# Kernel optimization log

Hardware: AMD Instinct MI355X
Metric: run time of the kernel (lower is better)

## Reference

```python
import jax, jax.numpy as jnp
import numpy as np

H = 16
D = 64
EPS = 1e-6

def _phi(x):
    # elu_feature_map: elu(x) + 1
    return jax.nn.elu(x) + 1.0

def setup_inputs() -> dict:
    key = jax.random.key(0)
    k1, k2, k3, k4 = jax.random.split(key, 4)
    B, N = 4, 4096
    query = jax.random.normal(k1, (B, N, H * D), dtype=jnp.float32)
    key_t = jax.random.normal(k2, (B, N, H * D), dtype=jnp.float32)
    value = jax.random.normal(k3, (B, N, H * D), dtype=jnp.float32)
    W_out = jax.random.normal(k4, (D, H * D), dtype=jnp.float32) * (1.0 / np.sqrt(H * D))
    b_out = jnp.zeros((D,), dtype=jnp.float32)
    return {"query": query, "key": key_t, "value": value, "W_out": W_out, "b_out": b_out}

def reference(query, key, value, W_out, b_out):
    B, N, _ = query.shape
    # b n (h d) -> b h n d
    def split_heads(x):
        return x.reshape(B, N, H, D).transpose(0, 2, 1, 3)
    q = split_heads(query)
    k = split_heads(key)
    v = split_heads(value)
    Q = _phi(q)  # [B,H,N,D]
    K = _phi(k)
    # KV aggregation: O(N D^2)
    KV = jnp.einsum('bhnd,bhnm->bhdm', K, v)          # [B,H,D,D]
    Ksum = K.sum(axis=2)                               # [B,H,D]
    Z = 1.0 / (jnp.einsum('bhnd,bhd->bhn', Q, Ksum) + EPS)  # [B,H,N]
    out = jnp.einsum('bhnd,bhdm,bhn->bhnm', Q, KV, Z)  # [B,H,N,D]
    # b h n d -> b n h d -> (b*n, h*d)
    out = out.transpose(0, 2, 1, 3).reshape(B * N, H * D)
    return out @ W_out.T + b_out
```

## Files before the change

kernel.cpp:

```cpp
#include <hip/hip_runtime.h>

#define B_  4
#define N_  4096
#define H_  16
#define BH_ 64
#define S_  16
#define EPS_ 1e-6f

#define NST_ 40
#define TSZ_ 2560
#define KOST_ 72

typedef _Float16 h2  __attribute__((ext_vector_type(2)));
typedef _Float16 h8  __attribute__((ext_vector_type(8)));
typedef float    f4v __attribute__((ext_vector_type(4)));

struct H2x2 { h2 a, b; };
struct H2x4 { h2 e[4]; };

__device__ __forceinline__ h8 ld_h8(const _Float16* p) {
    f4v r = *(const f4v*)p;
    return __builtin_bit_cast(h8, r);
}
__device__ __forceinline__ H2x4 ld_h2x4(const _Float16* p) {
    f4v r = *(const f4v*)p;
    return __builtin_bit_cast(H2x4, r);
}
__device__ __forceinline__ void st_h2x2(_Float16* p, h2 a, h2 b) {
    H2x2 t{a, b};
    *(float2*)p = __builtin_bit_cast(float2, t);
}
__device__ __forceinline__ float phi(float x) {
    return x > 0.0f ? x + 1.0f : __expf(x);
}
__device__ __forceinline__ float fdot2(h2 a, h2 b, float c) {
    return __builtin_amdgcn_fdot2(a, b, c, false);
}

__global__ __launch_bounds__(256) void k_zero(float* __restrict__ p) {
    p[(size_t)blockIdx.x * 256 + threadIdx.x] = 0.f;
}

__global__ __launch_bounds__(256, 4) void k_kvpart(const float* __restrict__ K,
                                                   const float* __restrict__ V,
                                                   float* __restrict__ KV,
                                                   float* __restrict__ Ksum) {
    const int s = blockIdx.x, h = blockIdx.y, b = blockIdx.z;
    const int t = threadIdx.x, wv = t >> 6, lane = t & 63;
    const int rp2 = t >> 4, c4 = t & 15;
    const int l15 = lane & 15;

    __shared__ __align__(16) _Float16 pool[2 * 2 * TSZ_];

    f4v k0r, k1r, v0r, v1r;
    const float* baseK = K + ((size_t)(b * N_ + s * 256) * 1024 + h * 64 + c4 * 4);
    const float* baseV = V + ((size_t)(b * N_ + s * 256) * 1024 + h * 64 + c4 * 4);

    auto LOADX = [&](int chunk) {
        const int ro = (chunk * 32 + 2 * rp2) * 1024;
        k0r = *(const f4v*)(baseK + ro);
        k1r = *(const f4v*)(baseK + ro + 1024);
        v0r = *(const f4v*)(baseV + ro);
        v1r = *(const f4v*)(baseV + ro + 1024);
    };
    auto STOREX = [&](int bf) {
        _Float16* Kt = pool + bf * (2 * TSZ_);
        _Float16* Vt = Kt + TSZ_;
        const int nn = 2 * rp2;
#pragma unroll
        for (int dj = 0; dj < 4; ++dj) {
            const int d = 4 * c4 + dj;
            h2 kk, vv;
            kk.x = (_Float16)phi(k0r[dj]); kk.y = (_Float16)phi(k1r[dj]);
            vv.x = (_Float16)v0r[dj];      vv.y = (_Float16)v1r[dj];
            *(h2*)&Kt[d * NST_ + nn] = kk;
            *(h2*)&Vt[d * NST_ + nn] = vv;
        }
    };

    f4v acc[4];
#pragma unroll
    for (int j = 0; j < 4; ++j) acc[j] = (f4v){0.f, 0.f, 0.f, 0.f};
    float ksum = 0.f;
    h2 one2; one2.x = (_Float16)1.0f; one2.y = (_Float16)1.0f;
    const int fo = (lane >> 4) * 8;

    auto COMPUTE = [&](int bf) {
        const _Float16* Kt = pool + bf * (2 * TSZ_);
        const _Float16* Vt = Kt + TSZ_;
        h8 a0 = ld_h8(&Kt[(16 * wv + l15) * NST_ + fo]);
#pragma unroll
        for (int j = 0; j < 4; ++j) {
            h8 b0 = ld_h8(&Vt[(16 * j + l15) * NST_ + fo]);
            acc[j] = __builtin_amdgcn_mfma_f32_16x16x32_f16(a0, b0, acc[j], 0, 0, 0);
        }
        if (wv == 0) {
#pragma unroll
            for (int q = 0; q < 4; ++q) {
                H2x4 x = ld_h2x4(&Kt[lane * NST_ + q * 8]);
#pragma unroll
                for (int i = 0; i < 4; ++i) ksum = fdot2(x.e[i], one2, ksum);
            }
        }
    };

    LOADX(0);
    STOREX(0);
    __syncthreads();
#pragma unroll
    for (int c = 0; c < 8; ++c) {
        if (c < 7) LOADX(c + 1);
        COMPUTE(c & 1);
        if (c < 7) {
            STOREX((c + 1) & 1);
            __syncthreads();
        }
    }

    const int bh = b * 16 + h;
    float* outp = KV + (size_t)bh * 4096;
#pragma unroll
    for (int j = 0; j < 4; ++j)
#pragma unroll
        for (int r = 0; r < 4; ++r) {
            const int d = 16 * wv + (lane >> 4) * 4 + r;
            const int m = 16 * j + l15;
            atomicAdd(&outp[d * 64 + m], acc[j][r]);
        }
    if (wv == 0) atomicAdd(&Ksum[(size_t)bh * 64 + lane], ksum);
}

__global__ __launch_bounds__(256, 4) void k_makeM(const float* __restrict__ KV,
                                                  const float* __restrict__ W,
                                                  _Float16* __restrict__ Mt) {
    const int bh = blockIdx.x, dq = blockIdx.y;
    const int h  = bh & 15;
    const int t  = threadIdx.x;

    __shared__ float KVs[16][68];
    __shared__ float Ws[64][68];

    const f4v* kv4 = (const f4v*)KV;
    const f4v* W4  = (const f4v*)W;

    {
        const int row = t >> 4, c4 = t & 15;
        *(f4v*)&KVs[row][c4 * 4] = kv4[(size_t)bh * 1024 + (dq * 16 + row) * 16 + c4];
    }
    for (int idx = t; idx < 1024; idx += 256) {
        const int wrow = idx >> 4, wc = idx & 15;
        *(f4v*)&Ws[wrow][wc * 4] = W4[(size_t)wrow * 256 + h * 16 + wc];
    }
    __syncthreads();

    const int j = t >> 2, dl = (t & 3) * 4;
    float acc[4] = {0.f, 0.f, 0.f, 0.f};
#pragma unroll 4
    for (int m4 = 0; m4 < 16; ++m4) {
        f4v wr  = *(const f4v*)&Ws[j][m4 * 4];
        f4v kv0 = *(const f4v*)&KVs[dl + 0][m4 * 4];
        f4v kv1 = *(const f4v*)&KVs[dl + 1][m4 * 4];
        f4v kv2 = *(const f4v*)&KVs[dl + 2][m4 * 4];
        f4v kv3 = *(const f4v*)&KVs[dl + 3][m4 * 4];
        acc[0] += wr[0] * kv0[0] + wr[1] * kv0[1] + wr[2] * kv0[2] + wr[3] * kv0[3];
        acc[1] += wr[0] * kv1[0] + wr[1] * kv1[1] + wr[2] * kv1[2] + wr[3] * kv1[3];
        acc[2] += wr[0] * kv2[0] + wr[1] * kv2[1] + wr[2] * kv2[2] + wr[3] * kv2[3];
        acc[3] += wr[0] * kv3[0] + wr[1] * kv3[1] + wr[2] * kv3[2] + wr[3] * kv3[3];
    }
    h2 lo, hi;
    lo.x = (_Float16)acc[0]; lo.y = (_Float16)acc[1];
    hi.x = (_Float16)acc[2]; hi.y = (_Float16)acc[3];
    H2x2 pk{lo, hi};
    *(float2*)&Mt[((size_t)bh * 64 + j) * 64 + dq * 16 + dl] =
        __builtin_bit_cast(float2, pk);
}

__global__ __launch_bounds__(256, 4) void k_out(const float* __restrict__ Q,
                                                const _Float16* __restrict__ Mtg,
                                                const float* __restrict__ Ksum,
                                                const float* __restrict__ bout,
                                                float* __restrict__ out) {
    const int nc = blockIdx.x, b = blockIdx.y;
    const int n0 = nc * 16;
    const int t = threadIdx.x, wv = t >> 6, lane = t & 63;
    const int rp16 = t >> 4, c4 = t & 15, l15 = lane & 15;

    __shared__ __align__(16) _Float16 pool[2 * 80 * KOST_];
    __shared__ float zz[16];
    __shared__ h2 Kss[2][32];

    f4v qr, mr0, mr1;
    float ksa = 0.f, ksb = 0.f;
    auto LOAD = [&](int hh) {
        const int bh = b * 16 + hh;
        qr = *(const f4v*)(Q + ((size_t)(b * N_ + n0 + rp16) * 1024 + hh * 64 + c4 * 4));
        const f4v* gm = (const f4v*)(Mtg + (size_t)bh * 4096);
        mr0 = gm[t];
        mr1 = gm[t + 256];
        if (t < 32) {
            ksa = Ksum[(size_t)bh * 64 + 2 * t];
            ksb = Ksum[(size_t)bh * 64 + 2 * t + 1];
        }
    };
    auto STORE = [&](int bf) {
        _Float16* Qp = pool + bf * (80 * KOST_);
        _Float16* Mt = Qp + 16 * KOST_;
        h2 p0, p1;
        p0.x = (_Float16)phi(qr[0]); p0.y = (_Float16)phi(qr[1]);
        p1.x = (_Float16)phi(qr[2]); p1.y = (_Float16)phi(qr[3]);
        st_h2x2(&Qp[rp16 * KOST_ + 4 * c4], p0, p1);
        *(f4v*)&Mt[(t >> 3) * KOST_ + (t & 7) * 8] = mr0;
        *(f4v*)&Mt[((t + 256) >> 3) * KOST_ + (t & 7) * 8] = mr1;
        if (t < 32) { h2 kk; kk.x = (_Float16)ksa; kk.y = (_Float16)ksb; Kss[bf][t] = kk; }
    };

    const int fo = (lane >> 4) * 8;
    float facc[4] = {0.f, 0.f, 0.f, 0.f};

    LOAD(0);
    STORE(0);

    for (int hh = 0; hh < 16; ++hh) {
        if (hh + 1 < 16) LOAD(hh + 1);
        __syncthreads();
        const int bf = hh & 1;
        const _Float16* Qp = pool + bf * (80 * KOST_);
        const _Float16* Mt = Qp + 16 * KOST_;

        if (t < 16) {
            float zp = 0.f;
#pragma unroll
            for (int c = 0; c < 8; ++c) {
                H2x4 x = ld_h2x4(&Qp[t * KOST_ + c * 8]);
#pragma unroll
                for (int i = 0; i < 4; ++i) zp = fdot2(x.e[i], Kss[bf][c * 4 + i], zp);
            }
            zz[t] = 1.0f / (zp + EPS_);
        }
        __syncthreads();

        f4v acc = (f4v){0.f, 0.f, 0.f, 0.f};
#pragma unroll
        for (int ks = 0; ks < 2; ++ks) {
            h8 a0 = ld_h8(&Qp[l15 * KOST_ + ks * 32 + fo]);
            h8 b0 = ld_h8(&Mt[(16 * wv + l15) * KOST_ + ks * 32 + fo]);
            acc = __builtin_amdgcn_mfma_f32_16x16x32_f16(a0, b0, acc, 0, 0, 0);
        }
#pragma unroll
        for (int r = 0; r < 4; ++r) {
            const int row = (lane >> 4) * 4 + r;
            facc[r] += zz[row] * acc[r];
        }
        if (hh + 1 < 16) STORE((hh + 1) & 1);
    }

    const int j = 16 * wv + l15;
    const float bj = bout[j];
#pragma unroll
    for (int r = 0; r < 4; ++r) {
        const int n = n0 + (lane >> 4) * 4 + r;
        out[(size_t)(b * N_ + n) * 64 + j] = bj + facc[r];
    }
}

extern "C" void kernel_launch(void* const* d_in, const int* in_sizes, int n_in,
                              void* d_out, int out_size, void* d_ws, size_t ws_size,
                              hipStream_t stream) {
    const float* q  = (const float*)d_in[0];
    const float* k  = (const float*)d_in[1];
    const float* v  = (const float*)d_in[2];
    const float* W  = (const float*)d_in[3];
    const float* bo = (const float*)d_in[4];
    float* out = (float*)d_out;

    float* ws   = (float*)d_ws;
    float* KV   = ws;
    float* Ksum = KV + (size_t)BH_ * 4096;
    float* Mt   = Ksum + (size_t)BH_ * 64;

    k_zero<<<1040, 256, 0, stream>>>(KV);
    k_kvpart<<<dim3(S_, H_, B_), 256, 0, stream>>>(k, v, KV, Ksum);
    k_makeM<<<dim3(BH_, 4), 256, 0, stream>>>(KV, W, (_Float16*)Mt);
    k_out<<<dim3(N_ / 16, B_), 256, 0, stream>>>(q, (const _Float16*)Mt, Ksum, bo, out);
}
```

Baseline: 220.8 us.

## Fuse four kernels into one cooperative kernel with grid-wide syncs

```diff
diff --git a/kernel.cpp b/kernel.cpp
--- a/kernel.cpp
+++ b/kernel.cpp
@@ -1,4 +1,7 @@
 #include <hip/hip_runtime.h>
+#include <hip/hip_cooperative_groups.h>
+
+namespace cg = cooperative_groups;
 
 #define B_  4
 #define N_  4096
@@ -10,6 +13,7 @@
 #define NST_ 40
 #define TSZ_ 2560
 #define KOST_ 72
+#define POOLSZ_ (2 * 80 * KOST_)
 
 typedef _Float16 h2  __attribute__((ext_vector_type(2)));
 typedef _Float16 h8  __attribute__((ext_vector_type(8)));
@@ -37,20 +41,16 @@
     return __builtin_amdgcn_fdot2(a, b, c, false);
 }
 
-__global__ __launch_bounds__(256) void k_zero(float* __restrict__ p) {
-    p[(size_t)blockIdx.x * 256 + threadIdx.x] = 0.f;
-}
-
-__global__ __launch_bounds__(256, 4) void k_kvpart(const float* __restrict__ K,
-                                                   const float* __restrict__ V,
-                                                   float* __restrict__ KV,
-                                                   float* __restrict__ Ksum) {
-    const int s = blockIdx.x, h = blockIdx.y, b = blockIdx.z;
-    const int t = threadIdx.x, wv = t >> 6, lane = t & 63;
+
+__device__ __forceinline__ void phase_kvpart(int s, int h, int b, int t,
+                                             const float* __restrict__ K,
+                                             const float* __restrict__ V,
+                                             float* __restrict__ KV,
+                                             float* __restrict__ Ksum,
+                                             _Float16* pool) {
+    const int wv = t >> 6, lane = t & 63;
     const int rp2 = t >> 4, c4 = t & 15;
     const int l15 = lane & 15;
-
-    __shared__ __align__(16) _Float16 pool[2 * 2 * TSZ_];
 
     f4v k0r, k1r, v0r, v1r;
     const float* baseK = K + ((size_t)(b * N_ + s * 256) * 1024 + h * 64 + c4 * 4);
@@ -130,15 +130,14 @@
     if (wv == 0) atomicAdd(&Ksum[(size_t)bh * 64 + lane], ksum);
 }
 
-__global__ __launch_bounds__(256, 4) void k_makeM(const float* __restrict__ KV,
-                                                  const float* __restrict__ W,
-                                                  _Float16* __restrict__ Mt) {
-    const int bh = blockIdx.x, dq = blockIdx.y;
-    const int h  = bh & 15;
-    const int t  = threadIdx.x;
-
-    __shared__ float KVs[16][68];
-    __shared__ float Ws[64][68];
+__device__ __forceinline__ void phase_makeM(int bh, int dq, int t,
+                                            const float* __restrict__ KV,
+                                            const float* __restrict__ W,
+                                            _Float16* __restrict__ Mt,
+                                            float* fpool) {
+    float (*KVs)[68] = (float (*)[68])fpool;
+    float (*Ws)[68]  = (float (*)[68])(fpool + 16 * 68);
+    const int h = bh & 15;
 
     const f4v* kv4 = (const f4v*)KV;
     const f4v* W4  = (const f4v*)W;
@@ -175,19 +174,17 @@
         __builtin_bit_cast(float2, pk);
 }
 
-__global__ __launch_bounds__(256, 4) void k_out(const float* __restrict__ Q,
-                                                const _Float16* __restrict__ Mtg,
-                                                const float* __restrict__ Ksum,
-                                                const float* __restrict__ bout,
-                                                float* __restrict__ out) {
-    const int nc = blockIdx.x, b = blockIdx.y;
+__device__ __forceinline__ void phase_out(int nc, int b, int t,
+                                          const float* __restrict__ Q,
+                                          const _Float16* __restrict__ Mtg,
+                                          const float* __restrict__ Ksum,
+                                          const float* __restrict__ bout,
+                                          float* __restrict__ out,
+                                          _Float16* pool, float* zz,
+                                          h2 (*Kss)[32]) {
     const int n0 = nc * 16;
-    const int t = threadIdx.x, wv = t >> 6, lane = t & 63;
+    const int wv = t >> 6, lane = t & 63;
     const int rp16 = t >> 4, c4 = t & 15, l15 = lane & 15;
-
-    __shared__ __align__(16) _Float16 pool[2 * 80 * KOST_];
-    __shared__ float zz[16];
-    __shared__ h2 Kss[2][32];
 
     f4v qr, mr0, mr1;
     float ksa = 0.f, ksb = 0.f;
@@ -263,6 +260,65 @@
     }
 }
 
+__global__ __launch_bounds__(256, 4) void k_fused(const float* __restrict__ K,
+                                                  const float* __restrict__ V,
+                                                  const float* __restrict__ Q,
+                                                  const float* __restrict__ W,
+                                                  const float* __restrict__ bout,
+                                                  float* __restrict__ out,
+                                                  float* __restrict__ KV,
+                                                  float* __restrict__ Ksum,
+                                                  _Float16* __restrict__ Mt) {
+    const int bid = blockIdx.x;
+    const int t = threadIdx.x;
+    cg::grid_group grid = cg::this_grid();
+
+    __shared__ __align__(16) _Float16 pool[POOLSZ_];
+    __shared__ float zz[16];
+    __shared__ h2 Kss[2][32];
+
+    for (int idx = bid * 256 + t; idx < BH_ * 4096 + BH_ * 64; idx += 1024 * 256)
+        KV[idx] = 0.f;
+    grid.sync();
+
+    phase_kvpart(bid & 15, (bid >> 4) & 15, bid >> 8, t, K, V, KV, Ksum, pool);
+    __threadfence();
+    grid.sync();
+
+    if (bid < 256) phase_makeM(bid >> 2, bid & 3, t, KV, W, Mt, (float*)pool);
+    __threadfence();
+    grid.sync();
+
+    phase_out(bid & 255, bid >> 8, t, Q, Mt, Ksum, bout, out, pool, zz, Kss);
+}
+
+__global__ __launch_bounds__(256) void k_zero(float* __restrict__ p) {
+    p[(size_t)blockIdx.x * 256 + threadIdx.x] = 0.f;
+}
+__global__ __launch_bounds__(256, 4) void k_kvpart(const float* __restrict__ K,
+                                                   const float* __restrict__ V,
+                                                   float* __restrict__ KV,
+                                                   float* __restrict__ Ksum) {
+    __shared__ __align__(16) _Float16 pool[2 * 2 * TSZ_];
+    phase_kvpart(blockIdx.x, blockIdx.y, blockIdx.z, threadIdx.x, K, V, KV, Ksum, pool);
+}
+__global__ __launch_bounds__(256, 4) void k_makeM(const float* __restrict__ KV,
+                                                  const float* __restrict__ W,
+                                                  _Float16* __restrict__ Mt) {
+    __shared__ __align__(16) float fpool[80 * 68];
+    phase_makeM(blockIdx.x, blockIdx.y, threadIdx.x, KV, W, Mt, fpool);
+}
+__global__ __launch_bounds__(256, 4) void k_out(const float* __restrict__ Q,
+                                                const _Float16* __restrict__ Mtg,
+                                                const float* __restrict__ Ksum,
+                                                const float* __restrict__ bout,
+                                                float* __restrict__ out) {
+    __shared__ __align__(16) _Float16 pool[POOLSZ_];
+    __shared__ float zz[16];
+    __shared__ h2 Kss[2][32];
+    phase_out(blockIdx.x, blockIdx.y, threadIdx.x, Q, Mtg, Ksum, bout, out, pool, zz, Kss);
+}
+
 extern "C" void kernel_launch(void* const* d_in, const int* in_sizes, int n_in,
                               void* d_out, int out_size, void* d_ws, size_t ws_size,
                               hipStream_t stream) {
@@ -276,10 +332,17 @@
     float* ws   = (float*)d_ws;
     float* KV   = ws;
     float* Ksum = KV + (size_t)BH_ * 4096;
-    float* Mt   = Ksum + (size_t)BH_ * 64;
-
-    k_zero<<<1040, 256, 0, stream>>>(KV);
-    k_kvpart<<<dim3(S_, H_, B_), 256, 0, stream>>>(k, v, KV, Ksum);
-    k_makeM<<<dim3(BH_, 4), 256, 0, stream>>>(KV, W, (_Float16*)Mt);
-    k_out<<<dim3(N_ / 16, B_), 256, 0, stream>>>(q, (const _Float16*)Mt, Ksum, bo, out);
-}
+    _Float16* Mt = (_Float16*)(Ksum + (size_t)BH_ * 64);
+
+    void* args[] = {(void*)&k, (void*)&v, (void*)&q, (void*)&W, (void*)&bo,
+                    (void*)&out, (void*)&KV, (void*)&Ksum, (void*)&Mt};
+    hipError_t err = hipLaunchCooperativeKernel((const void*)k_fused,
+                                                dim3(1024), dim3(256),
+                                                args, 0, stream);
+    if (err != hipSuccess) {
+        k_zero<<<1040, 256, 0, stream>>>(KV);
+        k_kvpart<<<dim3(S_, H_, B_), 256, 0, stream>>>(k, v, KV, Ksum);
+        k_makeM<<<dim3(BH_, 4), 256, 0, stream>>>(KV, W, Mt);
+        k_out<<<dim3(N_ / 16, B_), 256, 0, stream>>>(q, Mt, Ksum, bo, out);
+    }
+}
```

New measurement: 667.3 us. +202.2%, slower.
